# Optimization experiments

Hardware: AMD Instinct MI355X
Metric: run time of the kernel (lower is better)

Reference implementation:

```python
import jax, jax.numpy as jnp
import numpy as np
import math

B, T, C, H, DFF = 4, 2048, 1024, 16, 4096
HD = C // H
EPS = 1e-5


def _layernorm(x, g, b):
    mu = jnp.mean(x, axis=-1, keepdims=True)
    var = jnp.var(x, axis=-1, keepdims=True)
    return (x - mu) * jax.lax.rsqrt(var + EPS) * g + b


def _new_gelu(x):
    # 0.5*x*(1+tanh(sqrt(2/pi)*(x+0.044715*x^3)))
    c = math.sqrt(2.0 / math.pi)
    return 0.5 * x * (1.0 + jnp.tanh(c * (x + 0.044715 * x ** 3)))


def setup_inputs() -> dict:
    key = jax.random.key(0)
    ks = jax.random.split(key, 12)
    s = lambda fan_in: 1.0 / math.sqrt(fan_in)
    return {
        "x": jax.random.normal(ks[0], (B, T, C), jnp.float32),
        "ln1_g": jnp.ones((C,), jnp.float32),
        "ln1_b": jnp.zeros((C,), jnp.float32),
        "w_qkv": jax.random.normal(ks[1], (C, 3 * C), jnp.float32) * s(C),
        "b_qkv": jnp.zeros((3 * C,), jnp.float32),
        "w_o": jax.random.normal(ks[2], (C, C), jnp.float32) * s(C),
        "b_o": jnp.zeros((C,), jnp.float32),
        "ln2_g": jnp.ones((C,), jnp.float32),
        "ln2_b": jnp.zeros((C,), jnp.float32),
        "w_fc": jax.random.normal(ks[3], (C, DFF), jnp.float32) * s(C),
        "b_fc": jnp.zeros((DFF,), jnp.float32),
        "w_proj": jax.random.normal(ks[4], (DFF, C), jnp.float32) * s(DFF),
        "b_proj": jnp.zeros((C,), jnp.float32),
    }


def reference(x, ln1_g, ln1_b, w_qkv, b_qkv, w_o, b_o, ln2_g, ln2_b, w_fc, b_fc, w_proj, b_proj):
    # --- attention sub-block ---
    h = _layernorm(x, ln1_g, ln1_b)
    qkv = h @ w_qkv + b_qkv                                  # (B,T,3C)
    q, k, v = jnp.split(qkv, 3, axis=-1)
    q = q.reshape(B, T, H, HD).transpose(0, 2, 1, 3)          # (B,H,T,hd)
    k = k.reshape(B, T, H, HD).transpose(0, 2, 1, 3)
    v = v.reshape(B, T, H, HD).transpose(0, 2, 1, 3)
    scores = jnp.einsum("bhqd,bhkd->bhqk", q, k) / math.sqrt(HD)
    causal = jnp.tril(jnp.ones((T, T), jnp.bool_))            # (T,T)
    scores = jnp.where(causal[None, None], scores, -jnp.inf)
    probs = jax.nn.softmax(scores, axis=-1)
    attn = jnp.einsum("bhqk,bhkd->bhqd", probs, v)
    attn = attn.transpose(0, 2, 1, 3).reshape(B, T, C)
    x = x + attn @ w_o + b_o
    # --- MLP sub-block ---
    h2 = _layernorm(x, ln2_g, ln2_b)
    x = x + _new_gelu(h2 @ w_fc + b_fc) @ w_proj + b_proj
    return x
```

## Files before the change

kernel.cpp:

```cpp
#include <hip/hip_runtime.h>
#include <hip/hip_bf16.h>

using bf16 = __hip_bfloat16;
typedef __attribute__((ext_vector_type(8))) short bf16x8;
typedef __attribute__((ext_vector_type(4))) float f32x4;
typedef __attribute__((ext_vector_type(16))) float f32x16;

#define LOG2E 1.4426950408889634f

__device__ inline short f2b(float f) {
  __hip_bfloat16 h = __float2bfloat16(f);
  return *reinterpret_cast<short*>(&h);
}
__device__ inline float b2f(short s) {
  unsigned int u = ((unsigned int)(unsigned short)s) << 16;
  float f;
  __builtin_memcpy(&f, &u, 4);
  return f;
}
__device__ inline unsigned pk2(float a, float b) {
  return (unsigned)(unsigned short)f2b(a) |
         ((unsigned)(unsigned short)f2b(b) << 16);
}

__global__ __launch_bounds__(256) void transpose_cast_kernel(
    const float* __restrict__ in, bf16* __restrict__ out, int K, int N) {
  __shared__ float tile[32][33];
  int tx = threadIdx.x & 31;
  int ty = threadIdx.x >> 5;
  int n0 = blockIdx.x * 32, k0 = blockIdx.y * 32;
#pragma unroll
  for (int i = 0; i < 4; i++)
    tile[ty + i * 8][tx] = in[(size_t)(k0 + ty + i * 8) * N + n0 + tx];
  __syncthreads();
#pragma unroll
  for (int i = 0; i < 4; i++)
    out[(size_t)(n0 + ty + i * 8) * K + k0 + tx] =
        __float2bfloat16(tile[tx][ty + i * 8]);
}

__global__ __launch_bounds__(256) void transpose_v_kernel(
    const bf16* __restrict__ qkv, bf16* __restrict__ vt) {
  __shared__ short tile[64][66];
  const int bh = blockIdx.y;
  const int b = bh >> 4, h = bh & 15;
  const int t0 = blockIdx.x * 64;
  const int tid = threadIdx.x;
  const int r = tid >> 3, c8 = (tid & 7) * 8;
#pragma unroll
  for (int p = 0; p < 2; p++) {
    int t = r + p * 32;
    bf16x8 v = *(const bf16x8*)&qkv[(size_t)(b * 2048 + t0 + t) * 3072 + 2048 +
                                    h * 64 + c8];
#pragma unroll
    for (int i = 0; i < 8; i++) tile[t][c8 + i] = v[i];
  }
  __syncthreads();
#pragma unroll
  for (int p = 0; p < 2; p++) {
    int d = r + p * 32;
    int tt = c8;
    bf16x8 o;
#pragma unroll
    for (int i = 0; i < 8; i++) o[i] = tile[tt + i][d];
    *(bf16x8*)&vt[(size_t)(bh * 64 + d) * 2048 + t0 + tt] = o;
  }
}

__global__ __launch_bounds__(256) void ln_kernel(
    const float* __restrict__ x, const float* __restrict__ g,
    const float* __restrict__ b, bf16* __restrict__ out) {
  int row = blockIdx.x;
  const float4 v = ((const float4*)(x + (size_t)row * 1024))[threadIdx.x];
  float s = v.x + v.y + v.z + v.w;
  float ss = v.x * v.x + v.y * v.y + v.z * v.z + v.w * v.w;
#pragma unroll
  for (int off = 1; off < 64; off <<= 1) {
    s += __shfl_xor(s, off);
    ss += __shfl_xor(ss, off);
  }
  __shared__ float red[2][4];
  int w = threadIdx.x >> 6, lane = threadIdx.x & 63;
  if (lane == 0) { red[0][w] = s; red[1][w] = ss; }
  __syncthreads();
  s = red[0][0] + red[0][1] + red[0][2] + red[0][3];
  ss = red[1][0] + red[1][1] + red[1][2] + red[1][3];
  float mu = s * (1.0f / 1024.0f);
  float var = ss * (1.0f / 1024.0f) - mu * mu;
  float rstd = rsqrtf(var + 1e-5f);
  const float4 gv = ((const float4*)g)[threadIdx.x];
  const float4 bv = ((const float4*)b)[threadIdx.x];
  short4 o4;
  o4.x = f2b((v.x - mu) * rstd * gv.x + bv.x);
  o4.y = f2b((v.y - mu) * rstd * gv.y + bv.y);
  o4.z = f2b((v.z - mu) * rstd * gv.z + bv.z);
  o4.w = f2b((v.w - mu) * rstd * gv.w + bv.w);
  ((short4*)out)[(size_t)row * 256 + threadIdx.x] = o4;
}

__global__ __launch_bounds__(256) void fused_ln_kernel(
    const float* __restrict__ p0, const float* __restrict__ p1,
    const float* __restrict__ bo, const float* __restrict__ x,
    const float* __restrict__ g, const float* __restrict__ bln,
    float* __restrict__ x1, bf16* __restrict__ h2) {
  int row = blockIdx.x;
  size_t base = (size_t)row * 256 + threadIdx.x;
  float4 a = ((const float4*)p0)[base];
  float4 c = ((const float4*)p1)[base];
  float4 xr = ((const float4*)x)[base];
  float4 bo4 = ((const float4*)bo)[threadIdx.x];
  float4 v;
  v.x = a.x + c.x + xr.x + bo4.x;
  v.y = a.y + c.y + xr.y + bo4.y;
  v.z = a.z + c.z + xr.z + bo4.z;
  v.w = a.w + c.w + xr.w + bo4.w;
  ((float4*)x1)[base] = v;
  float s = v.x + v.y + v.z + v.w;
  float ss = v.x * v.x + v.y * v.y + v.z * v.z + v.w * v.w;
#pragma unroll
  for (int off = 1; off < 64; off <<= 1) {
    s += __shfl_xor(s, off);
    ss += __shfl_xor(ss, off);
  }
  __shared__ float red[2][4];
  int w = threadIdx.x >> 6, lane = threadIdx.x & 63;
  if (lane == 0) { red[0][w] = s; red[1][w] = ss; }
  __syncthreads();
  s = red[0][0] + red[0][1] + red[0][2] + red[0][3];
  ss = red[1][0] + red[1][1] + red[1][2] + red[1][3];
  float mu = s * (1.0f / 1024.0f);
  float var = ss * (1.0f / 1024.0f) - mu * mu;
  float rstd = rsqrtf(var + 1e-5f);
  const float4 gv = ((const float4*)g)[threadIdx.x];
  const float4 bv = ((const float4*)bln)[threadIdx.x];
  short4 o4;
  o4.x = f2b((v.x - mu) * rstd * gv.x + bv.x);
  o4.y = f2b((v.y - mu) * rstd * gv.y + bv.y);
  o4.z = f2b((v.z - mu) * rstd * gv.z + bv.z);
  o4.w = f2b((v.w - mu) * rstd * gv.w + bv.w);
  ((short4*)h2)[base] = o4;
}

__global__ __launch_bounds__(256) void fused_add_kernel(
    float* __restrict__ out, const float* __restrict__ q1,
    const float* __restrict__ x1, const float* __restrict__ bp, int n4) {
  for (int i = blockIdx.x * 256 + threadIdx.x; i < n4; i += gridDim.x * 256) {
    float4 a = ((const float4*)out)[i];
    float4 c = ((const float4*)q1)[i];
    float4 xr = ((const float4*)x1)[i];
    float4 b4 = ((const float4*)bp)[i & 255];
    float4 v;
    v.x = a.x + c.x + xr.x + b4.x;
    v.y = a.y + c.y + xr.y + b4.y;
    v.z = a.z + c.z + xr.z + b4.z;
    v.w = a.w + c.w + xr.w + b4.w;
    ((float4*)out)[i] = v;
  }
}

template <int EPI>
__global__ __launch_bounds__(512, 1) void gemm256_kernel(
    const bf16* __restrict__ A, const bf16* __restrict__ Bt,
    const float* __restrict__ bias, float* __restrict__ out0,
    float* __restrict__ out1, void* __restrict__ outv, int M, int N, int Kfull,
    int Ksub, int ntiles) {
  __shared__ short As[2][256 * 64];
  __shared__ short Bs[2][256 * 64];
  const int tid = threadIdx.x;
  const int lane = tid & 63, wid = tid >> 6;
  const int wr = wid >> 2, wc = wid & 3;

  const int nwg = gridDim.x;
  const int flat = blockIdx.x;
  const int sw = (flat & 7) * (nwg >> 3) + (flat >> 3);
  const int kq = sw / ntiles;
  const int tile = sw % ntiles;
  const int gy = M >> 8;
  const int bcol = tile / gy, brow = tile % gy;
  const int koff = kq * Ksub;
  const int nk = Ksub >> 6;

  const int srow = tid >> 3;
  const int schs = (tid & 7) ^ (srow & 7);

  const bf16* gA[4];
  const bf16* gB[4];
  int dstL[4];
#pragma unroll
  for (int r = 0; r < 4; r++) {
    gA[r] = A + (size_t)(brow * 256 + r * 64 + srow) * Kfull + koff + schs * 8;
    gB[r] = Bt + (size_t)(bcol * 256 + r * 64 + srow) * Kfull + koff + schs * 8;
    dstL[r] = (r * 64 + wid * 8) * 64;
  }

  auto stA_half = [&](int kt, int buf, int hf) {
#pragma unroll
    for (int rr = 0; rr < 2; rr++) {
      const int r = hf * 2 + rr;
      __builtin_amdgcn_global_load_lds(
          (const __attribute__((address_space(1))) unsigned int*)(gA[r] +
                                                                  kt * 64),
          (__attribute__((address_space(3))) unsigned int*)&As[buf][dstL[r]],
          16, 0, 0);
    }
  };
  auto stB_half = [&](int kt, int buf, int hf) {
#pragma unroll
    for (int rr = 0; rr < 2; rr++) {
      const int r = hf * 2 + rr;
      __builtin_amdgcn_global_load_lds(
          (const __attribute__((address_space(1))) unsigned int*)(gB[r] +
                                                                  kt * 64),
          (__attribute__((address_space(3))) unsigned int*)&Bs[buf][dstL[r]],
          16, 0, 0);
    }
  };

  int ofA[2][4][2], ofB[2][2][2];
#pragma unroll
  for (int qm = 0; qm < 2; qm++)
#pragma unroll
    for (int mm = 0; mm < 4; mm++)
#pragma unroll
      for (int ks = 0; ks < 2; ks++) {
        int row = wr * 128 + qm * 64 + mm * 16 + (lane & 15);
        int ch = (ks * 4 + (lane >> 4)) ^ (row & 7);
        ofA[qm][mm][ks] = row * 64 + ch * 8;
      }
#pragma unroll
  for (int qn = 0; qn < 2; qn++)
#pragma unroll
    for (int nn = 0; nn < 2; nn++)
#pragma unroll
      for (int ks = 0; ks < 2; ks++) {
        int row = wc * 64 + qn * 32 + nn * 16 + (lane & 15);
        int ch = (ks * 4 + (lane >> 4)) ^ (row & 7);
        ofB[qn][nn][ks] = row * 64 + ch * 8;
      }

  f32x4 acc[8][4] = {};
  bf16x8 af[4][2], bf0[2][2], bf1[2][2];

  stA_half(0, 0, 0);
  stA_half(0, 0, 1);
  stB_half(0, 0, 0);
  stB_half(0, 0, 1);
  if (nk > 1) {
    stB_half(1, 1, 0);
    stB_half(1, 1, 1);
    asm volatile("s_waitcnt vmcnt(4)" ::: "memory");
  } else {
    asm volatile("s_waitcnt vmcnt(0)" ::: "memory");
  }
  __builtin_amdgcn_s_barrier();

  for (int t = 0; t < nk; t++) {
    const int cur = t & 1, nxt = cur ^ 1;
    const short* Ac = As[cur];
    const short* Bc = Bs[cur];
#pragma unroll
    for (int mm = 0; mm < 4; mm++)
#pragma unroll
      for (int ks = 0; ks < 2; ks++)
        af[mm][ks] = *(const bf16x8*)&Ac[ofA[0][mm][ks]];
#pragma unroll
    for (int nn = 0; nn < 2; nn++)
#pragma unroll
      for (int ks = 0; ks < 2; ks++)
        bf0[nn][ks] = *(const bf16x8*)&Bc[ofB[0][nn][ks]];
    if (t + 1 < nk) stA_half(t + 1, nxt, 0);
    __builtin_amdgcn_s_barrier();
    asm volatile("s_waitcnt lgkmcnt(0)" ::: "memory");
    __builtin_amdgcn_sched_barrier(0);
    __builtin_amdgcn_s_setprio(1);
#pragma unroll
    for (int mm = 0; mm < 4; mm++)
#pragma unroll
      for (int nn = 0; nn < 2; nn++)
#pragma unroll
        for (int ks = 0; ks < 2; ks++)
          acc[mm][nn] = __builtin_amdgcn_mfma_f32_16x16x32_bf16(
              af[mm][ks], bf0[nn][ks], acc[mm][nn], 0, 0, 0);
    __builtin_amdgcn_s_setprio(0);
    __builtin_amdgcn_s_barrier();
#pragma unroll
    for (int nn = 0; nn < 2; nn++)
#pragma unroll
      for (int ks = 0; ks < 2; ks++)
        bf1[nn][ks] = *(const bf16x8*)&Bc[ofB[1][nn][ks]];
    if (t + 1 < nk) stA_half(t + 1, nxt, 1);
    __builtin_amdgcn_s_barrier();
    asm volatile("s_waitcnt lgkmcnt(0)" ::: "memory");
    __builtin_amdgcn_sched_barrier(0);
    __builtin_amdgcn_s_setprio(1);
#pragma unroll
    for (int mm = 0; mm < 4; mm++)
#pragma unroll
      for (int nn = 0; nn < 2; nn++)
#pragma unroll
        for (int ks = 0; ks < 2; ks++)
          acc[mm][2 + nn] = __builtin_amdgcn_mfma_f32_16x16x32_bf16(
              af[mm][ks], bf1[nn][ks], acc[mm][2 + nn], 0, 0, 0);
    __builtin_amdgcn_s_setprio(0);
    __builtin_amdgcn_s_barrier();
#pragma unroll
    for (int mm = 0; mm < 4; mm++)
#pragma unroll
      for (int ks = 0; ks < 2; ks++)
        af[mm][ks] = *(const bf16x8*)&Ac[ofA[1][mm][ks]];
    if (t + 2 < nk) stB_half(t + 2, cur, 0);
    __builtin_amdgcn_s_barrier();
    asm volatile("s_waitcnt lgkmcnt(0)" ::: "memory");
    __builtin_amdgcn_sched_barrier(0);
    __builtin_amdgcn_s_setprio(1);
#pragma unroll
    for (int mm = 0; mm < 4; mm++)
#pragma unroll
      for (int nn = 0; nn < 2; nn++)
#pragma unroll
        for (int ks = 0; ks < 2; ks++)
          acc[4 + mm][2 + nn] = __builtin_amdgcn_mfma_f32_16x16x32_bf16(
              af[mm][ks], bf1[nn][ks], acc[4 + mm][2 + nn], 0, 0, 0);
    __builtin_amdgcn_s_setprio(0);
    __builtin_amdgcn_s_barrier();
    if (t + 2 < nk) stB_half(t + 2, cur, 1);
    __builtin_amdgcn_s_setprio(1);
#pragma unroll
    for (int mm = 0; mm < 4; mm++)
#pragma unroll
      for (int nn = 0; nn < 2; nn++)
#pragma unroll
        for (int ks = 0; ks < 2; ks++)
          acc[4 + mm][nn] = __builtin_amdgcn_mfma_f32_16x16x32_bf16(
              af[mm][ks], bf0[nn][ks], acc[4 + mm][nn], 0, 0, 0);
    __builtin_amdgcn_s_setprio(0);
    if (t + 2 < nk)
      asm volatile("s_waitcnt vmcnt(4)" ::: "memory");
    else if (t + 1 < nk)
      asm volatile("s_waitcnt vmcnt(0)" ::: "memory");
    __builtin_amdgcn_s_barrier();
  }

#pragma unroll
  for (int m = 0; m < 8; m++)
#pragma unroll
    for (int n = 0; n < 4; n++) {
      int gr0 = brow * 256 + wr * 128 + m * 16 + (lane >> 4) * 4;
      int gc = bcol * 256 + wc * 64 + n * 16 + (lane & 15);
      if constexpr (EPI == 3) {
        float* po = kq ? out1 : out0;
#pragma unroll
        for (int j = 0; j < 4; j++)
          po[(size_t)(gr0 + j) * N + gc] = acc[m][n][j];
      } else {
        float bia = bias[gc];
#pragma unroll
        for (int j = 0; j < 4; j++) {
          float v = acc[m][n][j] + bia;
          size_t idx = (size_t)(gr0 + j) * N + gc;
          if constexpr (EPI == 0) {
            ((bf16*)outv)[idx] = __float2bfloat16(v);
          } else {
            float u = 0.7978845608028654f * (v + 0.044715f * v * v * v);
            float t2 = exp2f(u * (2.0f * LOG2E));
            float th = 1.0f - 2.0f / (t2 + 1.0f);
            ((bf16*)outv)[idx] = __float2bfloat16(0.5f * v * (1.0f + th));
          }
        }
      }
    }
}

__global__ __launch_bounds__(256) void attn_kernel(
    const bf16* __restrict__ qkv, const bf16* __restrict__ vt,
    bf16* __restrict__ attn) {
  const int bh = blockIdx.x;
  const int qt = 15 - blockIdx.y;
  const int b = bh >> 4, h = bh & 15;
  const int tid = threadIdx.x, w = tid >> 6, lane = tid & 63;
  const int col = lane & 31;
  const int hi = lane >> 5;

  __shared__ short Kl[2][64 * 64];
  __shared__ short Vl[2][64 * 64];

  const int qbase = qt * 128 + w * 32;
  const int qglob = qbase + col;
  const size_t qrow = (size_t)(b * 2048 + qglob);

  bf16x8 qf[4];
#pragma unroll
  for (int dks = 0; dks < 4; dks++) {
    bf16x8 raw =
        *(const bf16x8*)&qkv[qrow * 3072 + h * 64 + dks * 16 + hi * 8];
#pragma unroll
    for (int i = 0; i < 8; i++) qf[dks][i] = f2b(b2f(raw[i]) * 0.125f);
  }

  auto stage = [&](int kt, int buf) {
    const int kv0s = kt * 64;
#pragma unroll
    for (int j = 0; j < 2; j++) {
      int c = (j * 4 + w) * 64 + lane;
      int row = c >> 3;
      int sw8 = ((c & 7) ^ (row & 7)) * 8;
      const bf16* gk =
          qkv + (size_t)(b * 2048 + kv0s + row) * 3072 + 1024 + h * 64 + sw8;
      __builtin_amdgcn_global_load_lds(
          (const __attribute__((address_space(1))) unsigned int*)gk,
          (__attribute__((address_space(3))) unsigned int*)(
              &Kl[buf][(j * 4 + w) * 512]),
          16, 0, 0);
      const bf16* gv = vt + (size_t)(bh * 64 + row) * 2048 + kv0s + sw8;
      __builtin_amdgcn_global_load_lds(
          (const __attribute__((address_space(1))) unsigned int*)gv,
          (__attribute__((address_space(3))) unsigned int*)(
              &Vl[buf][(j * 4 + w) * 512]),
          16, 0, 0);
    }
  };

  f32x16 ot[2] = {};
  float m = -1e30f, l = 0.0f;

  const int ktend = qt * 2 + 1;
  stage(0, 0);
  for (int kt = 0; kt <= ktend; kt++) {
    const int kv0 = kt * 64;
    const int cur = kt & 1;
    if (kt < ktend) {
      stage(kt + 1, cur ^ 1);
      asm volatile("s_waitcnt vmcnt(4)" ::: "memory");
    } else {
      asm volatile("s_waitcnt vmcnt(0)" ::: "memory");
    }
    __builtin_amdgcn_s_barrier();

    if (kv0 <= qbase + 31) {
      f32x16 st[2] = {};
#pragma unroll
      for (int s = 0; s < 2; s++) {
        int kvrow = s * 32 + col;
        int swz = kvrow & 7;
#pragma unroll
        for (int dks = 0; dks < 4; dks++) {
          int ch = (dks * 2 + hi) ^ swz;
          bf16x8 kf = *(const bf16x8*)&Kl[cur][kvrow * 64 + ch * 8];
          st[s] = __builtin_amdgcn_mfma_f32_32x32x16_bf16(kf, qf[dks], st[s],
                                                          0, 0, 0);
        }
      }
      if (kv0 + 63 > qbase) {
#pragma unroll
        for (int s = 0; s < 2; s++)
#pragma unroll
          for (int r = 0; r < 16; r++) {
            int kv = kv0 + s * 32 + (r & 3) + 8 * (r >> 2) + 4 * hi;
            if (kv > qglob) st[s][r] = -1e30f;
          }
      }
      float vm[16];
#pragma unroll
      for (int i = 0; i < 16; i++) vm[i] = fmaxf(st[0][i], st[1][i]);
#pragma unroll
      for (int w2 = 8; w2 >= 1; w2 >>= 1)
#pragma unroll
        for (int i = 0; i < w2; i++) vm[i] = fmaxf(vm[i], vm[i + w2]);
      float pmax = fmaxf(vm[0], __shfl_xor(vm[0], 32));
      if (!__all(pmax - m <= 8.0f)) {
        float mnew = fmaxf(m, pmax);
        float corr = exp2f((m - mnew) * LOG2E);
        m = mnew;
        l *= corr;
#pragma unroll
        for (int s = 0; s < 2; s++)
#pragma unroll
          for (int r = 0; r < 16; r++) ot[s][r] *= corr;
      }
#pragma unroll
      for (int s = 0; s < 2; s++)
#pragma unroll
        for (int r = 0; r < 16; r++)
          st[s][r] = exp2f((st[s][r] - m) * LOG2E);
      float vs[16];
#pragma unroll
      for (int i = 0; i < 16; i++) vs[i] = st[0][i] + st[1][i];
#pragma unroll
      for (int w2 = 8; w2 >= 1; w2 >>= 1)
#pragma unroll
        for (int i = 0; i < w2; i++) vs[i] += vs[i + w2];
      l += vs[0] + __shfl_xor(vs[0], 32);

#pragma unroll
      for (int sub = 0; sub < 2; sub++) {
#pragma unroll
        for (int kl = 0; kl < 2; kl++) {
          unsigned A0 = pk2(st[sub][kl * 8 + 0], st[sub][kl * 8 + 1]);
          unsigned A1 = pk2(st[sub][kl * 8 + 2], st[sub][kl * 8 + 3]);
          unsigned B0 = pk2(st[sub][kl * 8 + 4], st[sub][kl * 8 + 5]);
          unsigned B1 = pk2(st[sub][kl * 8 + 6], st[sub][kl * 8 + 7]);
          unsigned sA0 = (unsigned)__shfl_xor((int)A0, 32);
          unsigned sA1 = (unsigned)__shfl_xor((int)A1, 32);
          unsigned sB0 = (unsigned)__shfl_xor((int)B0, 32);
          unsigned sB1 = (unsigned)__shfl_xor((int)B1, 32);
          union { unsigned u[4]; bf16x8 v; } pf;
          pf.u[0] = hi ? sB0 : A0;
          pf.u[1] = hi ? sB1 : A1;
          pf.u[2] = hi ? B0 : sA0;
          pf.u[3] = hi ? B1 : sA1;
          int ks = sub * 2 + kl;
#pragma unroll
          for (int ds = 0; ds < 2; ds++) {
            int drow = ds * 32 + col;
            int ch = (ks * 2 + hi) ^ (drow & 7);
            bf16x8 vf = *(const bf16x8*)&Vl[cur][drow * 64 + ch * 8];
            ot[ds] = __builtin_amdgcn_mfma_f32_32x32x16_bf16(vf, pf.v, ot[ds],
                                                             0, 0, 0);
          }
        }
      }
    }
    __builtin_amdgcn_s_barrier();
  }

  float rl = 1.0f / l;
#pragma unroll
  for (int ds = 0; ds < 2; ds++)
#pragma unroll
    for (int j = 0; j < 4; j++) {
      ushort4 o4;
      o4.x = (unsigned short)f2b(ot[ds][4 * j + 0] * rl);
      o4.y = (unsigned short)f2b(ot[ds][4 * j + 1] * rl);
      o4.z = (unsigned short)f2b(ot[ds][4 * j + 2] * rl);
      o4.w = (unsigned short)f2b(ot[ds][4 * j + 3] * rl);
      *(ushort4*)&attn[qrow * 1024 + h * 64 + 32 * ds + 8 * j + 4 * hi] = o4;
    }
}

extern "C" void kernel_launch(void* const* d_in, const int* in_sizes, int n_in,
                              void* d_out, int out_size, void* d_ws,
                              size_t ws_size, hipStream_t stream) {
  (void)in_sizes; (void)n_in; (void)out_size; (void)ws_size;
  const float* x      = (const float*)d_in[0];
  const float* ln1_g  = (const float*)d_in[1];
  const float* ln1_b  = (const float*)d_in[2];
  const float* w_qkv  = (const float*)d_in[3];
  const float* b_qkv  = (const float*)d_in[4];
  const float* w_o    = (const float*)d_in[5];
  const float* b_o    = (const float*)d_in[6];
  const float* ln2_g  = (const float*)d_in[7];
  const float* ln2_b  = (const float*)d_in[8];
  const float* w_fc   = (const float*)d_in[9];
  const float* b_fc   = (const float*)d_in[10];
  const float* w_proj = (const float*)d_in[11];
  const float* b_proj = (const float*)d_in[12];
  float* out = (float*)d_out;

  char* ws = (char*)d_ws;
  const size_t MB = 1048576;
  float* x1     = (float*)(ws + 0);
  bf16* slotA   = (bf16*)(ws + 32 * MB);
  bf16* wt_qkv  = (bf16*)(ws + 48 * MB);
  bf16* wt_o    = (bf16*)(ws + 54 * MB);
  bf16* wt_fc   = (bf16*)(ws + 56 * MB);
  bf16* wt_proj = (bf16*)(ws + 64 * MB);
  bf16* qkvb    = (bf16*)(ws + 72 * MB);
  bf16* vtb     = (bf16*)(ws + 120 * MB);
  float* p0     = (float*)(ws + 72 * MB);
  float* p1     = (float*)(ws + 104 * MB);
  bf16* gbuf    = (bf16*)(ws + 72 * MB);
  float* q1     = (float*)(ws + 32 * MB);

  dim3 blk(256);
  transpose_cast_kernel<<<dim3(3072 / 32, 1024 / 32), blk, 0, stream>>>(
      w_qkv, wt_qkv, 1024, 3072);
  transpose_cast_kernel<<<dim3(1024 / 32, 1024 / 32), blk, 0, stream>>>(
      w_o, wt_o, 1024, 1024);
  transpose_cast_kernel<<<dim3(4096 / 32, 1024 / 32), blk, 0, stream>>>(
      w_fc, wt_fc, 1024, 4096);
  transpose_cast_kernel<<<dim3(1024 / 32, 4096 / 32), blk, 0, stream>>>(
      w_proj, wt_proj, 4096, 1024);

  ln_kernel<<<8192, blk, 0, stream>>>(x, ln1_g, ln1_b, slotA);
  gemm256_kernel<0><<<dim3(384), dim3(512), 0, stream>>>(
      slotA, wt_qkv, b_qkv, nullptr, nullptr, qkvb, 8192, 3072, 1024, 1024,
      384);
  transpose_v_kernel<<<dim3(32, 64), blk, 0, stream>>>(qkvb, vtb);
  attn_kernel<<<dim3(64, 16), blk, 0, stream>>>(qkvb, vtb, slotA);
  gemm256_kernel<3><<<dim3(256), dim3(512), 0, stream>>>(
      slotA, wt_o, nullptr, p0, p1, nullptr, 8192, 1024, 1024, 512, 128);
  fused_ln_kernel<<<8192, blk, 0, stream>>>(p0, p1, b_o, x, ln2_g, ln2_b, x1,
                                            slotA);
  gemm256_kernel<2><<<dim3(512), dim3(512), 0, stream>>>(
      slotA, wt_fc, b_fc, nullptr, nullptr, gbuf, 8192, 4096, 1024, 1024, 512);
  gemm256_kernel<3><<<dim3(256), dim3(512), 0, stream>>>(
      gbuf, wt_proj, nullptr, out, q1, nullptr, 8192, 1024, 4096, 2048, 128);
  fused_add_kernel<<<dim3(2048), blk, 0, stream>>>(out, q1, x1, b_proj,
                                                   2097152);
}
```

Before: 424.1 us.

## Fuse bias/residual into split-K GEMM epilogue, add 128-row FC GEMM, prescale log2e

The split-K output GEMMs now add bias and residual inside the first K-slice's epilogue, so the LN and final add kernels read one fewer full tensor. The FC+GELU GEMM moves to a new 128x256-tile kernel that uses single-buffered LDS and two blocks per CU, aiming for better occupancy and tail behavior. Attention folds log2(e) into the Q scaling so the exp2 arguments need no extra multiply. The new FC kernel lacks the double-buffered pipelining of the old kernel and may stall on loads.

```diff
diff --git a/kernel.cpp b/kernel.cpp
--- a/kernel.cpp
+++ b/kernel.cpp
@@ -100,20 +100,17 @@
 
 __global__ __launch_bounds__(256) void fused_ln_kernel(
     const float* __restrict__ p0, const float* __restrict__ p1,
-    const float* __restrict__ bo, const float* __restrict__ x,
     const float* __restrict__ g, const float* __restrict__ bln,
     float* __restrict__ x1, bf16* __restrict__ h2) {
   int row = blockIdx.x;
   size_t base = (size_t)row * 256 + threadIdx.x;
   float4 a = ((const float4*)p0)[base];
   float4 c = ((const float4*)p1)[base];
-  float4 xr = ((const float4*)x)[base];
-  float4 bo4 = ((const float4*)bo)[threadIdx.x];
   float4 v;
-  v.x = a.x + c.x + xr.x + bo4.x;
-  v.y = a.y + c.y + xr.y + bo4.y;
-  v.z = a.z + c.z + xr.z + bo4.z;
-  v.w = a.w + c.w + xr.w + bo4.w;
+  v.x = a.x + c.x;
+  v.y = a.y + c.y;
+  v.z = a.z + c.z;
+  v.w = a.w + c.w;
   ((float4*)x1)[base] = v;
   float s = v.x + v.y + v.z + v.w;
   float ss = v.x * v.x + v.y * v.y + v.z * v.z + v.w * v.w;
@@ -142,18 +139,15 @@
 }
 
 __global__ __launch_bounds__(256) void fused_add_kernel(
-    float* __restrict__ out, const float* __restrict__ q1,
-    const float* __restrict__ x1, const float* __restrict__ bp, int n4) {
+    float* __restrict__ out, const float* __restrict__ q1, int n4) {
   for (int i = blockIdx.x * 256 + threadIdx.x; i < n4; i += gridDim.x * 256) {
     float4 a = ((const float4*)out)[i];
     float4 c = ((const float4*)q1)[i];
-    float4 xr = ((const float4*)x1)[i];
-    float4 b4 = ((const float4*)bp)[i & 255];
     float4 v;
-    v.x = a.x + c.x + xr.x + b4.x;
-    v.y = a.y + c.y + xr.y + b4.y;
-    v.z = a.z + c.z + xr.z + b4.z;
-    v.w = a.w + c.w + xr.w + b4.w;
+    v.x = a.x + c.x;
+    v.y = a.y + c.y;
+    v.z = a.z + c.z;
+    v.w = a.w + c.w;
     ((float4*)out)[i] = v;
   }
 }
@@ -161,9 +155,9 @@
 template <int EPI>
 __global__ __launch_bounds__(512, 1) void gemm256_kernel(
     const bf16* __restrict__ A, const bf16* __restrict__ Bt,
-    const float* __restrict__ bias, float* __restrict__ out0,
-    float* __restrict__ out1, void* __restrict__ outv, int M, int N, int Kfull,
-    int Ksub, int ntiles) {
+    const float* __restrict__ bias, const float* __restrict__ res,
+    float* __restrict__ out0, float* __restrict__ out1,
+    void* __restrict__ outv, int M, int N, int Kfull, int Ksub, int ntiles) {
   __shared__ short As[2][256 * 64];
   __shared__ short Bs[2][256 * 64];
   const int tid = threadIdx.x;
@@ -347,11 +341,19 @@
     for (int n = 0; n < 4; n++) {
       int gr0 = brow * 256 + wr * 128 + m * 16 + (lane >> 4) * 4;
       int gc = bcol * 256 + wc * 64 + n * 16 + (lane & 15);
-      if constexpr (EPI == 3) {
-        float* po = kq ? out1 : out0;
-#pragma unroll
-        for (int j = 0; j < 4; j++)
-          po[(size_t)(gr0 + j) * N + gc] = acc[m][n][j];
+      if constexpr (EPI == 4) {
+        if (kq == 0) {
+          float bia = bias[gc];
+#pragma unroll
+          for (int j = 0; j < 4; j++) {
+            size_t idx = (size_t)(gr0 + j) * N + gc;
+            out0[idx] = acc[m][n][j] + bia + res[idx];
+          }
+        } else {
+#pragma unroll
+          for (int j = 0; j < 4; j++)
+            out1[(size_t)(gr0 + j) * N + gc] = acc[m][n][j];
+        }
       } else {
         float bia = bias[gc];
 #pragma unroll
@@ -371,6 +373,108 @@
     }
 }
 
+__global__ __launch_bounds__(512, 2) void gemm128b_kernel(
+    const bf16* __restrict__ A, const bf16* __restrict__ Bt,
+    const float* __restrict__ bias, bf16* __restrict__ out, int M, int N,
+    int K) {
+  __shared__ short As[128 * 64];
+  __shared__ short Bs[256 * 64];
+  const int tid = threadIdx.x;
+  const int lane = tid & 63, wid = tid >> 6;
+  const int wr = wid >> 2, wc = wid & 3;
+
+  const int nwg = gridDim.x;
+  const int flat = blockIdx.x;
+  const int sw = (flat & 7) * (nwg >> 3) + (flat >> 3);
+  const int gy = M >> 7;
+  const int bcol = sw / gy, brow = sw % gy;
+  const int nk = K >> 6;
+
+  const int srow = tid >> 3;
+  const int schs = (tid & 7) ^ (srow & 7);
+
+  int ofA[4][2], ofB[4][2];
+#pragma unroll
+  for (int mm = 0; mm < 4; mm++)
+#pragma unroll
+    for (int ks = 0; ks < 2; ks++) {
+      int row = wr * 64 + mm * 16 + (lane & 15);
+      int ch = (ks * 4 + (lane >> 4)) ^ (row & 7);
+      ofA[mm][ks] = row * 64 + ch * 8;
+    }
+#pragma unroll
+  for (int nn = 0; nn < 4; nn++)
+#pragma unroll
+    for (int ks = 0; ks < 2; ks++) {
+      int row = wc * 64 + nn * 16 + (lane & 15);
+      int ch = (ks * 4 + (lane >> 4)) ^ (row & 7);
+      ofB[nn][ks] = row * 64 + ch * 8;
+    }
+
+  f32x4 acc[4][4] = {};
+
+  for (int t = 0; t < nk; t++) {
+    __syncthreads();
+#pragma unroll
+    for (int r = 0; r < 2; r++) {
+      const bf16* src =
+          A + (size_t)(brow * 128 + r * 64 + srow) * K + t * 64 + schs * 8;
+      __builtin_amdgcn_global_load_lds(
+          (const __attribute__((address_space(1))) unsigned int*)src,
+          (__attribute__((address_space(3))) unsigned int*)
+              &As[(r * 64 + wid * 8) * 64],
+          16, 0, 0);
+    }
+#pragma unroll
+    for (int r = 0; r < 4; r++) {
+      const bf16* src =
+          Bt + (size_t)(bcol * 256 + r * 64 + srow) * K + t * 64 + schs * 8;
+      __builtin_amdgcn_global_load_lds(
+          (const __attribute__((address_space(1))) unsigned int*)src,
+          (__attribute__((address_space(3))) unsigned int*)
+              &Bs[(r * 64 + wid * 8) * 64],
+          16, 0, 0);
+    }
+    __syncthreads();
+    bf16x8 bfr[4][2];
+#pragma unroll
+    for (int nn = 0; nn < 4; nn++)
+#pragma unroll
+      for (int ks = 0; ks < 2; ks++)
+        bfr[nn][ks] = *(const bf16x8*)&Bs[ofB[nn][ks]];
+#pragma unroll
+    for (int mm = 0; mm < 4; mm++) {
+      bf16x8 af0 = *(const bf16x8*)&As[ofA[mm][0]];
+      bf16x8 af1 = *(const bf16x8*)&As[ofA[mm][1]];
+#pragma unroll
+      for (int nn = 0; nn < 4; nn++) {
+        acc[mm][nn] = __builtin_amdgcn_mfma_f32_16x16x32_bf16(
+            af0, bfr[nn][0], acc[mm][nn], 0, 0, 0);
+        acc[mm][nn] = __builtin_amdgcn_mfma_f32_16x16x32_bf16(
+            af1, bfr[nn][1], acc[mm][nn], 0, 0, 0);
+      }
+    }
+  }
+
+#pragma unroll
+  for (int m = 0; m < 4; m++)
+#pragma unroll
+    for (int n = 0; n < 4; n++) {
+      int gr0 = brow * 128 + wr * 64 + m * 16 + (lane >> 4) * 4;
+      int gc = bcol * 256 + wc * 64 + n * 16 + (lane & 15);
+      float bia = bias[gc];
+#pragma unroll
+      for (int j = 0; j < 4; j++) {
+        float v = acc[m][n][j] + bia;
+        float u = 0.7978845608028654f * (v + 0.044715f * v * v * v);
+        float t2 = exp2f(u * (2.0f * LOG2E));
+        float th = 1.0f - 2.0f / (t2 + 1.0f);
+        out[(size_t)(gr0 + j) * N + gc] =
+            __float2bfloat16(0.5f * v * (1.0f + th));
+      }
+    }
+}
+
 __global__ __launch_bounds__(256) void attn_kernel(
     const bf16* __restrict__ qkv, const bf16* __restrict__ vt,
     bf16* __restrict__ attn) {
@@ -394,7 +498,8 @@
     bf16x8 raw =
         *(const bf16x8*)&qkv[qrow * 3072 + h * 64 + dks * 16 + hi * 8];
 #pragma unroll
-    for (int i = 0; i < 8; i++) qf[dks][i] = f2b(b2f(raw[i]) * 0.125f);
+    for (int i = 0; i < 8; i++)
+      qf[dks][i] = f2b(b2f(raw[i]) * (0.125f * LOG2E));
   }
 
   auto stage = [&](int kt, int buf) {
@@ -469,7 +574,7 @@
       float pmax = fmaxf(vm[0], __shfl_xor(vm[0], 32));
       if (!__all(pmax - m <= 8.0f)) {
         float mnew = fmaxf(m, pmax);
-        float corr = exp2f((m - mnew) * LOG2E);
+        float corr = exp2f(m - mnew);
         m = mnew;
         l *= corr;
 #pragma unroll
@@ -480,8 +585,7 @@
 #pragma unroll
       for (int s = 0; s < 2; s++)
 #pragma unroll
-        for (int r = 0; r < 16; r++)
-          st[s][r] = exp2f((st[s][r] - m) * LOG2E);
+        for (int r = 0; r < 16; r++) st[s][r] = exp2f(st[s][r] - m);
       float vs[16];
 #pragma unroll
       for (int i = 0; i < 16; i++) vs[i] = st[0][i] + st[1][i];
@@ -583,18 +687,17 @@
 
   ln_kernel<<<8192, blk, 0, stream>>>(x, ln1_g, ln1_b, slotA);
   gemm256_kernel<0><<<dim3(384), dim3(512), 0, stream>>>(
-      slotA, wt_qkv, b_qkv, nullptr, nullptr, qkvb, 8192, 3072, 1024, 1024,
-      384);
+      slotA, wt_qkv, b_qkv, nullptr, nullptr, nullptr, qkvb, 8192, 3072, 1024,
+      1024, 384);
   transpose_v_kernel<<<dim3(32, 64), blk, 0, stream>>>(qkvb, vtb);
   attn_kernel<<<dim3(64, 16), blk, 0, stream>>>(qkvb, vtb, slotA);
-  gemm256_kernel<3><<<dim3(256), dim3(512), 0, stream>>>(
-      slotA, wt_o, nullptr, p0, p1, nullptr, 8192, 1024, 1024, 512, 128);
-  fused_ln_kernel<<<8192, blk, 0, stream>>>(p0, p1, b_o, x, ln2_g, ln2_b, x1,
-                                            slotA);
-  gemm256_kernel<2><<<dim3(512), dim3(512), 0, stream>>>(
-      slotA, wt_fc, b_fc, nullptr, nullptr, gbuf, 8192, 4096, 1024, 1024, 512);
-  gemm256_kernel<3><<<dim3(256), dim3(512), 0, stream>>>(
-      gbuf, wt_proj, nullptr, out, q1, nullptr, 8192, 1024, 4096, 2048, 128);
-  fused_add_kernel<<<dim3(2048), blk, 0, stream>>>(out, q1, x1, b_proj,
-                                                   2097152);
-}
+  gemm256_kernel<4><<<dim3(256), dim3(512), 0, stream>>>(
+      slotA, wt_o, b_o, x, p0, p1, nullptr, 8192, 1024, 1024, 512, 128);
+  fused_ln_kernel<<<8192, blk, 0, stream>>>(p0, p1, ln2_g, ln2_b, x1, slotA);
+  gemm128b_kernel<<<dim3(1024), dim3(512), 0, stream>>>(
+      slotA, wt_fc, b_fc, gbuf, 8192, 4096, 1024);
+  gemm256_kernel<4><<<dim3(256), dim3(512), 0, stream>>>(
+      gbuf, wt_proj, b_proj, x1, out, q1, nullptr, 8192, 1024, 4096, 2048,
+      128);
+  fused_add_kernel<<<dim3(2048), blk, 0, stream>>>(out, q1, 2097152);
+}
```

Result: no change. 425.6 us (+0.4%).
